# Kernel optimization log

Hardware: AMD Instinct MI355X
Metric: run time of the kernel (lower is better)

Reference implementation:

```python
import jax, jax.numpy as jnp
import numpy as np

D_K = 128
D_V = 128
SEQ_LEN = 2048


def setup_inputs() -> dict:
    key = jax.random.key(0)
    kq, kk, kv = jax.random.split(key, 3)
    q = jax.random.normal(kq, (SEQ_LEN, D_K), dtype=jnp.float32)
    k = jax.random.normal(kk, (SEQ_LEN, D_K), dtype=jnp.float32)
    v = jax.random.normal(kv, (SEQ_LEN, D_V), dtype=jnp.float32)
    return {"q": q, "k": k, "v": v}


def _step(carry, qkv):
    J, Svv, Sqv, Sqq, l = carry
    q, k, v = qkv
    l = l + 1
    fl = l.astype(J.dtype)
    # update_correlations: running means of outer products
    Svv = (fl - 1.0) / fl * Svv + jnp.outer(v, v) / fl
    Sqv = (fl - 1.0) / fl * Sqv + jnp.outer(q, v) / fl
    Sqq = (fl - 1.0) / fl * Sqq + jnp.outer(q, q) / fl

    first = l == 1

    # ecological params (J: [d_v, d_k], Sqv: [d_k, d_v], Sqq: [d_k, d_k])
    s_J = jnp.einsum('vk,kv->', J, Sqv)            # trace(J @ Sigma_qv)
    s_l = k @ Sqv @ v
    A_JJ = jnp.einsum('vk,kj,vj->', J, Sqq, J)     # trace(J Sqq J^T)
    A_ll = (v @ v) * (k @ Sqq @ k)
    A_Jl = v @ J @ Sqq @ k

    # safe denominators (unused branches must not produce NaN under where)
    A_JJ_s = jnp.where(first | (A_JJ == 0), 1.0, A_JJ)
    A_ll_s = jnp.where(first | (A_ll == 0), 1.0, A_ll)
    denom = A_JJ * A_ll - A_Jl ** 2
    denom_s = jnp.where(first | (denom == 0), 1.0, denom)

    margin = s_l - A_Jl * (s_J / A_JJ_s)

    wf = (A_ll * s_J - A_Jl * s_l) / denom_s
    wi = (A_JJ * s_l - A_Jl * s_J) / denom_s
    # nonnegativity constraints (check omega_i first, as in the source)
    wf_c = jnp.where(wi <= 0, s_J / A_JJ_s, jnp.where(wf <= 0, 0.0, wf))
    wi_c = jnp.where(wi <= 0, 0.0, jnp.where(wf <= 0, s_l / A_ll_s, wi))

    do_update = margin > 0
    vk = jnp.outer(v, k)
    J_upd = jnp.where(do_update, wf_c * J + wi_c * vk, J)
    J_new = jnp.where(first, vk, J_upd)
    updated = first | do_update

    # compute_cost with updated J and correlations
    cost = (0.5 * jnp.trace(Svv)
            - jnp.einsum('vk,kv->', J_new, Sqv)
            + 0.5 * jnp.einsum('vk,kj,vj->', J_new, Sqq, J_new))

    return (J_new, Svv, Sqv, Sqq, l), (cost, updated)


def _run(q, k, v):
    d_k, d_v = q.shape[-1], v.shape[-1]
    init = (jnp.zeros((d_v, d_k), q.dtype),
            jnp.zeros((d_v, d_v), q.dtype),
            jnp.zeros((d_k, d_v), q.dtype),
            jnp.zeros((d_k, d_k), q.dtype),
            jnp.int32(0))
    (J, _, _, _, _), (costs, updated) = jax.lax.scan(_step, init, (q, k, v))
    return costs, updated, J


def reference(q, k, v):
    return _run(q, k, v)
```

## Files before the change

### kernel.cpp

```cpp
#include <hip/hip_runtime.h>

#define SEQ 2048
#define D 128

typedef float v2f __attribute__((ext_vector_type(2)));
typedef float v4f __attribute__((ext_vector_type(4)));
#define LO2(v) __builtin_shufflevector(v, v, 0, 1)
#define HI2(v) __builtin_shufflevector(v, v, 2, 3)

__global__ __launch_bounds__(256) void precompute_kernel(
    const float* __restrict__ q, const float* __restrict__ k, const float* __restrict__ v,
    float* __restrict__ U, float* __restrict__ sl, float* __restrict__ kqq,
    float* __restrict__ vv, float* __restrict__ kq_adj, float* __restrict__ vv_adj,
    float* __restrict__ kU_adj, double* __restrict__ invl)
{
    const int s = blockIdx.x;
    const int tid = threadIdx.x;

    __shared__ float ks[D];
    __shared__ float vs[D];
    __shared__ float alpha[SEQ];
    __shared__ float red[8];
    __shared__ float upart[256];

    if (tid < D) ks[tid] = k[s * D + tid];
    else if (tid < 2 * D) vs[tid - D] = v[s * D + (tid - D)];
    __syncthreads();

    float p_a2 = 0.f, p_ab = 0.f;
    for (int i = tid; i <= s; i += 256) {
        const float4* qr = (const float4*)(q + (size_t)i * D);
        const float4* vr = (const float4*)(v + (size_t)i * D);
        float a = 0.f, b = 0.f;
#pragma unroll
        for (int j = 0; j < D / 4; ++j) {
            float4 q4 = qr[j];
            float4 v4 = vr[j];
            a += q4.x * ks[4 * j + 0] + q4.y * ks[4 * j + 1] + q4.z * ks[4 * j + 2] + q4.w * ks[4 * j + 3];
            b += v4.x * vs[4 * j + 0] + v4.y * vs[4 * j + 1] + v4.z * vs[4 * j + 2] + v4.w * vs[4 * j + 3];
        }
        alpha[i] = a;
        p_a2 += a * a;
        p_ab += a * b;
        if (i == s) vv[s] = b;
    }
#pragma unroll
    for (int off = 1; off < 64; off <<= 1) {
        p_a2 += __shfl_xor(p_a2, off);
        p_ab += __shfl_xor(p_ab, off);
    }
    const int wid = tid >> 6;
    if ((tid & 63) == 0) { red[wid] = p_a2; red[4 + wid] = p_ab; }
    __syncthreads();
    if (tid == 0) {
        kqq[s] = red[0] + red[1] + red[2] + red[3];
        sl[s]  = red[4] + red[5] + red[6] + red[7];
        invl[s] = 1.0 / (double)(s + 1);
    }

    if (tid < 64) {
        if (s + 1 < SEQ) {
            float p2 = ks[tid] * q[(size_t)(s + 1) * D + tid]
                     + ks[tid + 64] * q[(size_t)(s + 1) * D + 64 + tid];
#pragma unroll
            for (int off = 1; off < 64; off <<= 1) p2 += __shfl_xor(p2, off);
            if (tid == 0) kq_adj[s + 1] = p2;
        }
        if (s == 0 && tid == 0) { kq_adj[0] = 0.f; kU_adj[0] = 0.f; vv_adj[0] = 0.f; }
    } else if (tid < 128 && s > 0) {
        const int t2 = tid - 64;
        float p2 = vs[t2] * v[(size_t)(s - 1) * D + t2]
                 + vs[t2 + 64] * v[(size_t)(s - 1) * D + 64 + t2];
#pragma unroll
        for (int off = 1; off < 64; off <<= 1) p2 += __shfl_xor(p2, off);
        if (t2 == 0) vv_adj[s] = p2;
    }

    const int c = tid & (D - 1);
    const int h = tid >> 7;
    float a0 = 0.f, a1 = 0.f, a2 = 0.f, a3 = 0.f;
    int i = h;
    for (; i + 6 <= s; i += 8) {
        a0 = fmaf(q[(size_t)(i    ) * D + c], alpha[i    ], a0);
        a1 = fmaf(q[(size_t)(i + 2) * D + c], alpha[i + 2], a1);
        a2 = fmaf(q[(size_t)(i + 4) * D + c], alpha[i + 4], a2);
        a3 = fmaf(q[(size_t)(i + 6) * D + c], alpha[i + 6], a3);
    }
    for (; i <= s; i += 2) a0 = fmaf(q[(size_t)i * D + c], alpha[i], a0);
    upart[tid] = (a0 + a1) + (a2 + a3);
    __syncthreads();

    float kup = 0.f;
    if (tid < D) {
        const float uv = upart[tid] + upart[tid + D];
        U[(size_t)s * D + tid] = uv;
        if (s > 0) kup = uv * k[(size_t)(s - 1) * D + tid];
    }
#pragma unroll
    for (int off = 1; off < 64; off <<= 1) kup += __shfl_xor(kup, off);
    if (tid == 0)  red[0] = kup;
    if (tid == 64) red[1] = kup;
    __syncthreads();
    if (s > 0 && tid == 0) kU_adj[s] = red[0] + red[1];
}

#define DPP_ADD(x, ctrl) \
    ((x) + __int_as_float(__builtin_amdgcn_update_dpp(0, __float_as_int(x), (ctrl), 0xf, 0xf, true)))
#define REDUCE16(x) do { x = DPP_ADD(x, 0xB1); x = DPP_ADD(x, 0x4E); \
                         x = DPP_ADD(x, 0x141); x = DPP_ADD(x, 0x140); } while (0)

#define BARRIER() do { asm volatile("s_waitcnt lgkmcnt(0)" ::: "memory"); \
                       __builtin_amdgcn_s_barrier(); } while (0)

#define UPDATE_J(MODE, WF, WI)                                                \
    if ((MODE) == 2) {                                                        \
        const v2f wA = {vc4.x, vc4.x}, wB = {vc4.y, vc4.y};                   \
        const v2f wC = {vc4.z, vc4.z}, wD = {vc4.w, vc4.w};                   \
        jA0 = wA * k0_; jA1 = wA * k1_; jA2 = wA * k2_; jA3 = wA * k3_;       \
        jB0 = wB * k0_; jB1 = wB * k1_; jB2 = wB * k2_; jB3 = wB * k3_;       \
        jC0 = wC * k0_; jC1 = wC * k1_; jC2 = wC * k2_; jC3 = wC * k3_;       \
        jD0 = wD * k0_; jD1 = wD * k1_; jD2 = wD * k2_; jD3 = wD * k3_;       \
    } else if ((MODE) == 1) {                                                 \
        const v2f wf2 = {(WF), (WF)};                                         \
        const float sA = (WI) * vc4.x, sB = (WI) * vc4.y;                     \
        const float sC = (WI) * vc4.z, sD = (WI) * vc4.w;                     \
        const v2f wA = {sA, sA}, wB = {sB, sB}, wC = {sC, sC}, wD = {sD, sD}; \
        jA0 = __builtin_elementwise_fma(jA0, wf2, wA * k0_);                  \
        jA1 = __builtin_elementwise_fma(jA1, wf2, wA * k1_);                  \
        jA2 = __builtin_elementwise_fma(jA2, wf2, wA * k2_);                  \
        jA3 = __builtin_elementwise_fma(jA3, wf2, wA * k3_);                  \
        jB0 = __builtin_elementwise_fma(jB0, wf2, wB * k0_);                  \
        jB1 = __builtin_elementwise_fma(jB1, wf2, wB * k1_);                  \
        jB2 = __builtin_elementwise_fma(jB2, wf2, wB * k2_);                  \
        jB3 = __builtin_elementwise_fma(jB3, wf2, wB * k3_);                  \
        jC0 = __builtin_elementwise_fma(jC0, wf2, wC * k0_);                  \
        jC1 = __builtin_elementwise_fma(jC1, wf2, wC * k1_);                  \
        jC2 = __builtin_elementwise_fma(jC2, wf2, wC * k2_);                  \
        jC3 = __builtin_elementwise_fma(jC3, wf2, wC * k3_);                  \
        jD0 = __builtin_elementwise_fma(jD0, wf2, wD * k0_);                  \
        jD1 = __builtin_elementwise_fma(jD1, wf2, wD * k1_);                  \
        jD2 = __builtin_elementwise_fma(jD2, wf2, wD * k2_);                  \
        jD3 = __builtin_elementwise_fma(jD3, wf2, wD * k3_);                  \
    }

__global__ __launch_bounds__(1024, 4) void scan_kernel(
    const float* __restrict__ q, const float* __restrict__ k, const float* __restrict__ v,
    const float* __restrict__ U, const float* __restrict__ sl_arr,
    const float* __restrict__ kqq_arr, const float* __restrict__ vv_arr,
    const float* __restrict__ kq_adj, const float* __restrict__ vv_adj,
    const float* __restrict__ kU_adj, const double* __restrict__ invl_arr,
    float* __restrict__ out)
{
    const int tid  = threadIdx.x;
    const int lane = tid & 63;
    const int w    = __builtin_amdgcn_readfirstlane(tid >> 6);

    __shared__ float ring[3][4][160];
    __shared__ __align__(16) float wred[3][32][4];
    __shared__ __align__(16) float decLDS[3][4];

    const bool isj     = (tid >= 512);
    const int  jw      = w - 8;
    const int  i16     = lane & 15;
    const int  r4      = lane >> 4;
    const int  o       = 20 * (i16 >> 1) + 8 * (i16 & 1);
    const int  rb      = (jw << 4) + (r4 << 2);
    const int  vo      = 20 * jw + (r4 << 2);

    const bool stager  = (tid >= 128) && (tid < 512);
    const int  which   = (tid >> 7) - 1;
    const int  sidx    = tid & 127;
    const int  widx    = ((sidx >> 4) * 20) + (sidx & 15);

    const bool vstager = (tid >= 64) && (tid < 128);
    const int  s2      = tid & 63;
    const int  vc0     = 2 * s2;
    const int  vwidx   = 20 * (vc0 >> 4) + (vc0 & 15);

    v2f jA0 = {0.f, 0.f}, jA1 = jA0, jA2 = jA0, jA3 = jA0;
    v2f jB0 = jA0, jB1 = jA0, jB2 = jA0, jB3 = jA0;
    v2f jC0 = jA0, jC1 = jA0, jC2 = jA0, jC3 = jA0;
    v2f jD0 = jA0, jD1 = jA0, jD2 = jA0, jD3 = jA0;
    v4f vc4 = {0.f, 0.f, 0.f, 0.f}, vn4 = vc4;

    float gs[3] = {0.f, 0.f, 0.f};
    v2f   gv[3] = {{0.f,0.f},{0.f,0.f},{0.f,0.f}};
    float p_sl[3] = {0,0,0}, p_kq[3] = {0,0,0}, p_vv[3] = {0,0,0};
    float p_kqa[3] = {0,0,0}, p_vva[3] = {0,0,0}, p_vvp[3] = {0,0,0};
    float p_kua[3] = {0,0,0};
    double p_inv[3] = {0,0,0};

    if (stager) {
        if (which == 0) {
            ring[0][0][widx] = q[(size_t)1 * D + sidx];
            ring[1][0][widx] = q[(size_t)2 * D + sidx];
            gs[2] = q[(size_t)3 * D + sidx];
            gs[0] = q[(size_t)4 * D + sidx];
            gs[1] = q[(size_t)5 * D + sidx];
        } else if (which == 1) {
            ring[0][1][widx] = U[(size_t)1 * D + sidx];
            ring[1][1][widx] = U[(size_t)2 * D + sidx];
            gs[2] = U[(size_t)3 * D + sidx];
            gs[0] = U[(size_t)4 * D + sidx];
            gs[1] = U[(size_t)5 * D + sidx];
        } else {
            ring[0][2][widx] = k[sidx];
            ring[1][2][widx] = k[(size_t)1 * D + sidx];
            gs[2] = k[(size_t)2 * D + sidx];
            gs[0] = k[(size_t)3 * D + sidx];
            gs[1] = k[(size_t)4 * D + sidx];
        }
    } else if (vstager) {
        *(v2f*)&ring[0][3][vwidx] = *(const v2f*)&v[(size_t)1 * D + vc0];
        *(v2f*)&ring[1][3][vwidx] = *(const v2f*)&v[(size_t)2 * D + vc0];
        gv[2] = *(const v2f*)&v[(size_t)3 * D + vc0];
        gv[0] = *(const v2f*)&v[(size_t)4 * D + vc0];
        gv[1] = *(const v2f*)&v[(size_t)5 * D + vc0];
    } else if (isj) {
        vc4 = *(const v4f*)&v[rb];
    }

    float dwf = 0.f, dwi = 1.f;
    int dmode = 2;
    if (tid == 0) { decLDS[0][0] = 0.f; decLDS[0][1] = 1.f; decLDS[0][2] = 2.f; decLDS[0][3] = 0.f; }

    double SJ = 0.0, AJJ = 0.0, trSvv = 0.0;
    if (w == 0) {
        p_sl[0]  = sl_arr[1];  p_kq[0]  = kqq_arr[1]; p_vv[0] = vv_arr[1];
        p_kqa[0] = kq_adj[1];  p_vva[0] = vv_adj[1];  p_kua[0] = kU_adj[1];
        p_inv[0] = invl_arr[1]; p_vvp[0] = vv_arr[0];
        p_sl[1]  = sl_arr[2];  p_kq[1]  = kqq_arr[2]; p_vv[1] = vv_arr[2];
        p_kqa[1] = kq_adj[2];  p_vva[1] = vv_adj[2];  p_kua[1] = kU_adj[2];
        p_inv[1] = invl_arr[2]; p_vvp[1] = vv_arr[1];

        const double sl0 = (double)sl_arr[0];
        const double kq0 = (double)kqq_arr[0];
        const double vv0 = (double)vv_arr[0];
        trSvv = vv0;
        SJ  = sl0;
        AJJ = vv0 * kq0;
        if (lane == 0) {
            out[0] = (float)((0.5 * trSvv - SJ + 0.5 * AJJ) * invl_arr[0]);
            out[SEQ] = 1.f;
        }
    }
    BARRIER();

#define STEP_BODY(I, P, PN, PW)                                               \
{                                                                             \
    v2f k0_ = {0.f, 0.f}, k1_ = k0_, k2_ = k0_, k3_ = k0_;                    \
    if (isj) {                                                                \
        const v4f Qa = ((const v4f*)&ring[P][0][o])[0];                       \
        const v4f Qb = ((const v4f*)&ring[P][0][o])[1];                       \
        const v4f Ua = ((const v4f*)&ring[P][1][o])[0];                       \
        const v4f Ub = ((const v4f*)&ring[P][1][o])[1];                       \
        const v4f Ka = ((const v4f*)&ring[P][2][o])[0];                       \
        const v4f Kb = ((const v4f*)&ring[P][2][o])[1];                       \
        vn4 = *((const v4f*)&ring[P][3][vo]);                                 \
        k0_ = LO2(Ka); k1_ = HI2(Ka); k2_ = LO2(Kb); k3_ = HI2(Kb);           \
        const v2f q0 = LO2(Qa), q1 = HI2(Qa), q2 = LO2(Qb), q3 = HI2(Qb);     \
        v2f aA = jA0 * q0, aB = jB0 * q0, aC = jC0 * q0, aD = jD0 * q0;       \
        aA = __builtin_elementwise_fma(jA1, q1, aA);                          \
        aB = __builtin_elementwise_fma(jB1, q1, aB);                          \
        aC = __builtin_elementwise_fma(jC1, q1, aC);                          \
        aD = __builtin_elementwise_fma(jD1, q1, aD);                          \
        aA = __builtin_elementwise_fma(jA2, q2, aA);                          \
        aB = __builtin_elementwise_fma(jB2, q2, aB);                          \
        aC = __builtin_elementwise_fma(jC2, q2, aC);                          \
        aD = __builtin_elementwise_fma(jD2, q2, aD);                          \
        aA = __builtin_elementwise_fma(jA3, q3, aA);                          \
        aB = __builtin_elementwise_fma(jB3, q3, aB);                          \
        aC = __builtin_elementwise_fma(jC3, q3, aC);                          \
        aD = __builtin_elementwise_fma(jD3, q3, aD);                          \
        float YqA = aA.x + aA.y, YqB = aB.x + aB.y;                           \
        float YqC = aC.x + aC.y, YqD = aD.x + aD.y;                           \
        const v2f u0 = LO2(Ua), u1 = HI2(Ua), u2 = LO2(Ub), u3 = HI2(Ub);     \
        v2f bA = jA0 * u0, bB = jB0 * u0, bC = jC0 * u0, bD = jD0 * u0;       \
        bA = __builtin_elementwise_fma(jA1, u1, bA);                          \
        bB = __builtin_elementwise_fma(jB1, u1, bB);                          \
        bC = __builtin_elementwise_fma(jC1, u1, bC);                          \
        bD = __builtin_elementwise_fma(jD1, u1, bD);                          \
        bA = __builtin_elementwise_fma(jA2, u2, bA);                          \
        bB = __builtin_elementwise_fma(jB2, u2, bB);                          \
        bC = __builtin_elementwise_fma(jC2, u2, bC);                          \
        bD = __builtin_elementwise_fma(jD2, u2, bD);                          \
        bA = __builtin_elementwise_fma(jA3, u3, bA);                          \
        bB = __builtin_elementwise_fma(jB3, u3, bB);                          \
        bC = __builtin_elementwise_fma(jC3, u3, bC);                          \
        bD = __builtin_elementwise_fma(jD3, u3, bD);                          \
        float YwA = bA.x + bA.y, YwB = bB.x + bB.y;                           \
        float YwC = bC.x + bC.y, YwD = bD.x + bD.y;                           \
        REDUCE16(YqA); REDUCE16(YqB); REDUCE16(YqC); REDUCE16(YqD);           \
        REDUCE16(YwA); REDUCE16(YwB); REDUCE16(YwC); REDUCE16(YwD);           \
        const float z1 = (vn4.x * YqA + vn4.y * YqB) + (vn4.z * YqC + vn4.w * YqD); \
        const float z2 = (YqA * YqA + YqB * YqB) + (YqC * YqC + YqD * YqD);   \
        const float z3 = (vc4.x * YqA + vc4.y * YqB) + (vc4.z * YqC + vc4.w * YqD); \
        const float z4 = (vn4.x * YwA + vn4.y * YwB) + (vn4.z * YwC + vn4.w * YwD); \
        if ((lane & 15) == 15)                                                \
            *(float4*)&wred[P][(jw << 2) | r4][0] = make_float4(z1, z2, z3, z4); \
    } else if (w == 0) {                                                      \
        const int t_ = ((I) + 3 < SEQ) ? (I) + 3 : SEQ - 1;                   \
        p_sl[PW]  = sl_arr[t_];   p_kq[PW]  = kqq_arr[t_];                    \
        p_vv[PW]  = vv_arr[t_];   p_kqa[PW] = kq_adj[t_];                     \
        p_vva[PW] = vv_adj[t_];   p_kua[PW] = kU_adj[t_];                     \
        p_inv[PW] = invl_arr[t_]; p_vvp[PW] = p_vv[PN];                       \
    }                                                                         \
    BARRIER();                                                                \
    if (stager) {                                                             \
        ring[PW][which][widx] = gs[PW];                                       \
        const int tq_ = ((I) + 6 < SEQ) ? (I) + 6 : SEQ - 1;                  \
        const int tk_ = ((I) + 5 < SEQ) ? (I) + 5 : SEQ - 1;                  \
        gs[PW] = (which == 0) ? q[(size_t)tq_ * D + sidx]                     \
               : (which == 1) ? U[(size_t)tq_ * D + sidx]                     \
                              : k[(size_t)tk_ * D + sidx];                    \
    } else if (vstager) {                                                     \
        *(v2f*)&ring[PW][3][vwidx] = gv[PW];                                  \
        const int tv_ = ((I) + 6 < SEQ) ? (I) + 6 : SEQ - 1;                  \
        gv[PW] = *(const v2f*)&v[(size_t)tv_ * D + vc0];                      \
    } else if (isj) {                                                         \
        const float4 df = *(const float4*)&decLDS[P][0];                      \
        const float uwf = df.x, uwi = df.y;                                   \
        const int   umode = (int)df.z;                                        \
        UPDATE_J(umode, uwf, uwi)                                             \
        vc4 = vn4;                                                            \
    } else if (w == 0) {                                                      \
        const float c_sl  = p_sl[P],  c_kq  = p_kq[P],  c_vv  = p_vv[P];      \
        const float c_kqa = p_kqa[P], c_vva = p_vva[P], c_vvp = p_vvp[P];     \
        const float c_kua = p_kua[P];                                         \
        const double c_inv = p_inv[P];                                        \
        const float4 wa = *(const float4*)&wred[P][lane & 15][0];             \
        const float4 wb = *(const float4*)&wred[P][16 + (lane & 15)][0];      \
        float4 ww = make_float4(wa.x + wb.x, wa.y + wb.y,                     \
                                wa.z + wb.z, wa.w + wb.w);                    \
        const float odwf = dwf, odwi = dwi;                                   \
        const int   odmode = dmode;                                           \
        REDUCE16(ww.x);                                                       \
        REDUCE16(ww.y);                                                       \
        REDUCE16(ww.z);                                                       \
        REDUCE16(ww.w);                                                       \
        double a_, b_;                                                        \
        if (odmode == 2)      { a_ = 0.0; b_ = 1.0; }                         \
        else if (odmode == 1) { a_ = (double)odwf; b_ = (double)odwi; }       \
        else                  { a_ = 1.0; b_ = 0.0; }                         \
        const double kqa = (double)c_kqa, vva = (double)c_vva;                \
        const double vvp = (double)c_vvp, kua = (double)c_kua;                \
        const double r1 = (double)ww.x, r2 = (double)ww.y;                    \
        const double r3 = (double)ww.z, r4_ = (double)ww.w;                   \
        const double Jqv  = a_ * r1 + b_ * (kqa * vva);                       \
        const double Jq2  = a_ * a_ * r2 + 2.0 * a_ * b_ * kqa * r3          \
                          + b_ * b_ * kqa * kqa * vvp;                        \
        const double AJl_ = a_ * r4_ + b_ * kua * vva;                        \
        trSvv += (double)c_vv;                                                \
        SJ    += Jqv;                                                         \
        AJJ   += Jq2;                                                         \
        const double s_l  = (double)c_sl;                                     \
        const double A_ll = (double)c_vv * (double)c_kq;                      \
        const double AJJ_s  = (AJJ == 0.0)  ? 1.0 : AJJ;                      \
        const double A_ll_s = (A_ll == 0.0) ? 1.0 : A_ll;                     \
        const double divJ = SJ / AJJ_s;     \
        const double divL = s_l / A_ll_s;   \
        const double denom   = AJJ * A_ll - AJl_ * AJl_;                      \
        const double denom_s = (denom == 0.0) ? 1.0 : denom;                  \
        const double rden = 1.0 / denom_s;                                    \
        const double wf = (A_ll * SJ - AJl_ * s_l) * rden;                    \
        const double wi = (AJJ * s_l - AJl_ * SJ) * rden;                     \
        double wf_c, wi_c;                                                    \
        if (wi <= 0.0)      { wf_c = divJ; wi_c = 0.0; }                      \
        else if (wf <= 0.0) { wf_c = 0.0;  wi_c = divL; }                     \
        else                { wf_c = wf;   wi_c = wi; }                       \
        const bool do_update = (s_l * AJJ_s - AJl_ * SJ) > 0.0;               \
        int mode;                                                             \
        if (do_update) {                                                      \
            mode = 1;                                                         \
            const double nSJ = wf_c * SJ + wi_c * s_l;                        \
            AJJ = wf_c * wf_c * AJJ + 2.0 * wf_c * wi_c * AJl_                \
                + wi_c * wi_c * A_ll;                                         \
            SJ = nSJ;                                                         \
        } else {                                                              \
            mode = 0;                                                         \
        }                                                                     \
        dwf = (float)wf_c; dwi = (float)wi_c; dmode = mode;                   \
        if (lane == 0) {                                                      \
            out[(I) + 1] = (float)((0.5 * trSvv - SJ + 0.5 * AJJ) * c_inv);   \
            out[SEQ + (I) + 1] = mode ? 1.f : 0.f;                            \
            *(float4*)&decLDS[PN][0] = make_float4(dwf, dwi, (float)mode, 0.f);\
        }                                                                     \
    }                                                                         \
}

    for (int i = 0; i + 2 < SEQ - 1; i += 3) {
        STEP_BODY(i,     0, 1, 2)
        STEP_BODY(i + 1, 1, 2, 0)
        STEP_BODY(i + 2, 2, 0, 1)
    }
    STEP_BODY(SEQ - 2, 0, 1, 2)
#undef STEP_BODY

    BARRIER();
    if (isj) {
        const float4 df = *(const float4*)&decLDS[1][0];
        const float fwf = df.x, fwi = df.y;
        const int   fmode = (int)df.z;
        const v4f Ka = ((const v4f*)&ring[1][2][o])[0];
        const v4f Kb = ((const v4f*)&ring[1][2][o])[1];
        const v2f k0_ = LO2(Ka), k1_ = HI2(Ka), k2_ = LO2(Kb), k3_ = HI2(Kb);
        UPDATE_J(fmode, fwf, fwi)
        float* jb = out + 2 * SEQ + (size_t)rb * D + 8 * i16;
        *(v4f*)(jb + 0)         = __builtin_shufflevector(jA0, jA1, 0, 1, 2, 3);
        *(v4f*)(jb + 4)         = __builtin_shufflevector(jA2, jA3, 0, 1, 2, 3);
        *(v4f*)(jb + D + 0)     = __builtin_shufflevector(jB0, jB1, 0, 1, 2, 3);
        *(v4f*)(jb + D + 4)     = __builtin_shufflevector(jB2, jB3, 0, 1, 2, 3);
        *(v4f*)(jb + 2 * D + 0) = __builtin_shufflevector(jC0, jC1, 0, 1, 2, 3);
        *(v4f*)(jb + 2 * D + 4) = __builtin_shufflevector(jC2, jC3, 0, 1, 2, 3);
        *(v4f*)(jb + 3 * D + 0) = __builtin_shufflevector(jD0, jD1, 0, 1, 2, 3);
        *(v4f*)(jb + 3 * D + 4) = __builtin_shufflevector(jD2, jD3, 0, 1, 2, 3);
    }
}

extern "C" void kernel_launch(void* const* d_in, const int* in_sizes, int n_in,
                              void* d_out, int out_size, void* d_ws, size_t ws_size,
                              hipStream_t stream) {
    (void)in_sizes; (void)n_in; (void)out_size; (void)ws_size;
    const float* q = (const float*)d_in[0];
    const float* k = (const float*)d_in[1];
    const float* v = (const float*)d_in[2];
    float* out = (float*)d_out;

    float* U      = (float*)d_ws;
    float* sl     = U + (size_t)SEQ * D;
    float* kqq    = sl + SEQ;
    float* vv     = kqq + SEQ;
    float* kq_adj = vv + SEQ;
    float* vv_adj = kq_adj + SEQ;
    float* kU_adj = vv_adj + SEQ;
    double* invl  = (double*)(kU_adj + SEQ);

    precompute_kernel<<<SEQ, 256, 0, stream>>>(q, k, v, U, sl, kqq, vv,
                                               kq_adj, vv_adj, kU_adj, invl);
    scan_kernel<<<1, 1024, 0, stream>>>(q, k, v, U, sl, kqq, vv,
                                        kq_adj, vv_adj, kU_adj, invl, out);
}
```

Before: 2.615 ms.

## Compute scalar decision redundantly in all J waves and update J immediately

Instead of wave 0 computing the per-step scalar decision and publishing it through LDS for the J waves to apply one step later, every J wave now reduces the partial sums itself, runs the double-precision decision, and applies the J update in the same step. The J update is applied eagerly, so the reductions already see the updated J and the adjustment terms (kq_adj, vv_adj, kU_adj) are dropped. The per-step scalar inputs are preloaded into LDS at kernel start, and a sched_barrier is added after each barrier. This removes a cross-wave handoff and one pipeline stage per step, at the cost of redundant double-precision math in all eight J waves and more LDS.

Result: no change. 2.606 ms (-0.3%).

```diff
diff --git a/kernel.cpp b/kernel.cpp
--- a/kernel.cpp
+++ b/kernel.cpp
@@ -110,38 +110,8 @@
                          x = DPP_ADD(x, 0x141); x = DPP_ADD(x, 0x140); } while (0)
 
 #define BARRIER() do { asm volatile("s_waitcnt lgkmcnt(0)" ::: "memory"); \
-                       __builtin_amdgcn_s_barrier(); } while (0)
-
-#define UPDATE_J(MODE, WF, WI)                                                \
-    if ((MODE) == 2) {                                                        \
-        const v2f wA = {vc4.x, vc4.x}, wB = {vc4.y, vc4.y};                   \
-        const v2f wC = {vc4.z, vc4.z}, wD = {vc4.w, vc4.w};                   \
-        jA0 = wA * k0_; jA1 = wA * k1_; jA2 = wA * k2_; jA3 = wA * k3_;       \
-        jB0 = wB * k0_; jB1 = wB * k1_; jB2 = wB * k2_; jB3 = wB * k3_;       \
-        jC0 = wC * k0_; jC1 = wC * k1_; jC2 = wC * k2_; jC3 = wC * k3_;       \
-        jD0 = wD * k0_; jD1 = wD * k1_; jD2 = wD * k2_; jD3 = wD * k3_;       \
-    } else if ((MODE) == 1) {                                                 \
-        const v2f wf2 = {(WF), (WF)};                                         \
-        const float sA = (WI) * vc4.x, sB = (WI) * vc4.y;                     \
-        const float sC = (WI) * vc4.z, sD = (WI) * vc4.w;                     \
-        const v2f wA = {sA, sA}, wB = {sB, sB}, wC = {sC, sC}, wD = {sD, sD}; \
-        jA0 = __builtin_elementwise_fma(jA0, wf2, wA * k0_);                  \
-        jA1 = __builtin_elementwise_fma(jA1, wf2, wA * k1_);                  \
-        jA2 = __builtin_elementwise_fma(jA2, wf2, wA * k2_);                  \
-        jA3 = __builtin_elementwise_fma(jA3, wf2, wA * k3_);                  \
-        jB0 = __builtin_elementwise_fma(jB0, wf2, wB * k0_);                  \
-        jB1 = __builtin_elementwise_fma(jB1, wf2, wB * k1_);                  \
-        jB2 = __builtin_elementwise_fma(jB2, wf2, wB * k2_);                  \
-        jB3 = __builtin_elementwise_fma(jB3, wf2, wB * k3_);                  \
-        jC0 = __builtin_elementwise_fma(jC0, wf2, wC * k0_);                  \
-        jC1 = __builtin_elementwise_fma(jC1, wf2, wC * k1_);                  \
-        jC2 = __builtin_elementwise_fma(jC2, wf2, wC * k2_);                  \
-        jC3 = __builtin_elementwise_fma(jC3, wf2, wC * k3_);                  \
-        jD0 = __builtin_elementwise_fma(jD0, wf2, wD * k0_);                  \
-        jD1 = __builtin_elementwise_fma(jD1, wf2, wD * k1_);                  \
-        jD2 = __builtin_elementwise_fma(jD2, wf2, wD * k2_);                  \
-        jD3 = __builtin_elementwise_fma(jD3, wf2, wD * k3_);                  \
-    }
+                       __builtin_amdgcn_s_barrier(); \
+                       __builtin_amdgcn_sched_barrier(0); } while (0)
 
 __global__ __launch_bounds__(1024, 4) void scan_kernel(
     const float* __restrict__ q, const float* __restrict__ k, const float* __restrict__ v,
@@ -154,10 +124,14 @@
     const int tid  = threadIdx.x;
     const int lane = tid & 63;
     const int w    = __builtin_amdgcn_readfirstlane(tid >> 6);
+    (void)kq_adj; (void)vv_adj; (void)kU_adj;
 
     __shared__ float ring[3][4][160];
     __shared__ __align__(16) float wred[3][32][4];
-    __shared__ __align__(16) float decLDS[3][4];
+    __shared__ __align__(16) float fsl[SEQ];
+    __shared__ __align__(16) float fkq[SEQ];
+    __shared__ __align__(16) float fvv[SEQ];
+    __shared__ __align__(16) double finv[SEQ];
 
     const bool isj     = (tid >= 512);
     const int  jw      = w - 8;
@@ -181,14 +155,17 @@
     v2f jB0 = jA0, jB1 = jA0, jB2 = jA0, jB3 = jA0;
     v2f jC0 = jA0, jC1 = jA0, jC2 = jA0, jC3 = jA0;
     v2f jD0 = jA0, jD1 = jA0, jD2 = jA0, jD3 = jA0;
-    v4f vc4 = {0.f, 0.f, 0.f, 0.f}, vn4 = vc4;
 
     float gs[3] = {0.f, 0.f, 0.f};
     v2f   gv[3] = {{0.f,0.f},{0.f,0.f},{0.f,0.f}};
-    float p_sl[3] = {0,0,0}, p_kq[3] = {0,0,0}, p_vv[3] = {0,0,0};
-    float p_kqa[3] = {0,0,0}, p_vva[3] = {0,0,0}, p_vvp[3] = {0,0,0};
-    float p_kua[3] = {0,0,0};
-    double p_inv[3] = {0,0,0};
+
+    if (tid < 512) {
+        ((float4*)fsl)[tid] = ((const float4*)sl_arr)[tid];
+        ((float4*)fvv)[tid] = ((const float4*)vv_arr)[tid];
+    } else {
+        ((float4*)fkq)[tid - 512] = ((const float4*)kqq_arr)[tid - 512];
+    }
+    ((double2*)finv)[tid] = ((const double2*)invl_arr)[tid];
 
     if (stager) {
         if (which == 0) {
@@ -204,11 +181,11 @@
             gs[0] = U[(size_t)4 * D + sidx];
             gs[1] = U[(size_t)5 * D + sidx];
         } else {
-            ring[0][2][widx] = k[sidx];
-            ring[1][2][widx] = k[(size_t)1 * D + sidx];
-            gs[2] = k[(size_t)2 * D + sidx];
-            gs[0] = k[(size_t)3 * D + sidx];
-            gs[1] = k[(size_t)4 * D + sidx];
+            ring[0][2][widx] = k[(size_t)1 * D + sidx];
+            ring[1][2][widx] = k[(size_t)2 * D + sidx];
+            gs[2] = k[(size_t)3 * D + sidx];
+            gs[0] = k[(size_t)4 * D + sidx];
+            gs[1] = k[(size_t)5 * D + sidx];
         }
     } else if (vstager) {
         *(v2f*)&ring[0][3][vwidx] = *(const v2f*)&v[(size_t)1 * D + vc0];
@@ -216,40 +193,43 @@
         gv[2] = *(const v2f*)&v[(size_t)3 * D + vc0];
         gv[0] = *(const v2f*)&v[(size_t)4 * D + vc0];
         gv[1] = *(const v2f*)&v[(size_t)5 * D + vc0];
-    } else if (isj) {
-        vc4 = *(const v4f*)&v[rb];
-    }
-
-    float dwf = 0.f, dwi = 1.f;
-    int dmode = 2;
-    if (tid == 0) { decLDS[0][0] = 0.f; decLDS[0][1] = 1.f; decLDS[0][2] = 2.f; decLDS[0][3] = 0.f; }
+    }
 
     double SJ = 0.0, AJJ = 0.0, trSvv = 0.0;
-    if (w == 0) {
-        p_sl[0]  = sl_arr[1];  p_kq[0]  = kqq_arr[1]; p_vv[0] = vv_arr[1];
-        p_kqa[0] = kq_adj[1];  p_vva[0] = vv_adj[1];  p_kua[0] = kU_adj[1];
-        p_inv[0] = invl_arr[1]; p_vvp[0] = vv_arr[0];
-        p_sl[1]  = sl_arr[2];  p_kq[1]  = kqq_arr[2]; p_vv[1] = vv_arr[2];
-        p_kqa[1] = kq_adj[2];  p_vva[1] = vv_adj[2];  p_kua[1] = kU_adj[2];
-        p_inv[1] = invl_arr[2]; p_vvp[1] = vv_arr[1];
-
+    if (isj) {
+        const v4f v0  = *(const v4f*)&v[rb];
+        const v4f Ka0 = *(const v4f*)&k[8 * i16];
+        const v4f Kb0 = *(const v4f*)&k[8 * i16 + 4];
+        const v2f k0_ = LO2(Ka0), k1_ = HI2(Ka0), k2_ = LO2(Kb0), k3_ = HI2(Kb0);
+        const v2f wA = {v0.x, v0.x}, wB = {v0.y, v0.y};
+        const v2f wC = {v0.z, v0.z}, wD = {v0.w, v0.w};
+        jA0 = wA * k0_; jA1 = wA * k1_; jA2 = wA * k2_; jA3 = wA * k3_;
+        jB0 = wB * k0_; jB1 = wB * k1_; jB2 = wB * k2_; jB3 = wB * k3_;
+        jC0 = wC * k0_; jC1 = wC * k1_; jC2 = wC * k2_; jC3 = wC * k3_;
+        jD0 = wD * k0_; jD1 = wD * k1_; jD2 = wD * k2_; jD3 = wD * k3_;
+        const double vv0 = (double)vv_arr[0];
+        SJ    = (double)sl_arr[0];
+        AJJ   = vv0 * (double)kqq_arr[0];
+        trSvv = vv0;
+    }
+    if (tid == 0) {
         const double sl0 = (double)sl_arr[0];
         const double kq0 = (double)kqq_arr[0];
         const double vv0 = (double)vv_arr[0];
-        trSvv = vv0;
-        SJ  = sl0;
-        AJJ = vv0 * kq0;
-        if (lane == 0) {
-            out[0] = (float)((0.5 * trSvv - SJ + 0.5 * AJJ) * invl_arr[0]);
-            out[SEQ] = 1.f;
-        }
-    }
-    BARRIER();
+        out[0] = (float)((0.5 * vv0 - sl0 + 0.5 * vv0 * kq0) * invl_arr[0]);
+        out[SEQ] = 1.f;
+    }
+    __syncthreads();
 
 #define STEP_BODY(I, P, PN, PW)                                               \
 {                                                                             \
+    float c_sl = 0.f, c_kq = 0.f, c_vv = 0.f;                                 \
+    double c_inv = 0.0;                                                       \
     v2f k0_ = {0.f, 0.f}, k1_ = k0_, k2_ = k0_, k3_ = k0_;                    \
+    v4f vn4 = {0.f, 0.f, 0.f, 0.f};                                           \
     if (isj) {                                                                \
+        c_sl = fsl[(I) + 1]; c_kq = fkq[(I) + 1]; c_vv = fvv[(I) + 1];        \
+        c_inv = finv[(I) + 1];                                                \
         const v4f Qa = ((const v4f*)&ring[P][0][o])[0];                       \
         const v4f Qb = ((const v4f*)&ring[P][0][o])[1];                       \
         const v4f Ua = ((const v4f*)&ring[P][1][o])[0];                       \
@@ -294,96 +274,83 @@
         REDUCE16(YwA); REDUCE16(YwB); REDUCE16(YwC); REDUCE16(YwD);           \
         const float z1 = (vn4.x * YqA + vn4.y * YqB) + (vn4.z * YqC + vn4.w * YqD); \
         const float z2 = (YqA * YqA + YqB * YqB) + (YqC * YqC + YqD * YqD);   \
-        const float z3 = (vc4.x * YqA + vc4.y * YqB) + (vc4.z * YqC + vc4.w * YqD); \
         const float z4 = (vn4.x * YwA + vn4.y * YwB) + (vn4.z * YwC + vn4.w * YwD); \
         if ((lane & 15) == 15)                                                \
-            *(float4*)&wred[P][(jw << 2) | r4][0] = make_float4(z1, z2, z3, z4); \
-    } else if (w == 0) {                                                      \
-        const int t_ = ((I) + 3 < SEQ) ? (I) + 3 : SEQ - 1;                   \
-        p_sl[PW]  = sl_arr[t_];   p_kq[PW]  = kqq_arr[t_];                    \
-        p_vv[PW]  = vv_arr[t_];   p_kqa[PW] = kq_adj[t_];                     \
-        p_vva[PW] = vv_adj[t_];   p_kua[PW] = kU_adj[t_];                     \
-        p_inv[PW] = invl_arr[t_]; p_vvp[PW] = p_vv[PN];                       \
+            *(float4*)&wred[P][(jw << 2) | r4][0] = make_float4(z1, z2, z4, 0.f); \
     }                                                                         \
     BARRIER();                                                                \
     if (stager) {                                                             \
         ring[PW][which][widx] = gs[PW];                                       \
-        const int tq_ = ((I) + 6 < SEQ) ? (I) + 6 : SEQ - 1;                  \
-        const int tk_ = ((I) + 5 < SEQ) ? (I) + 5 : SEQ - 1;                  \
-        gs[PW] = (which == 0) ? q[(size_t)tq_ * D + sidx]                     \
-               : (which == 1) ? U[(size_t)tq_ * D + sidx]                     \
-                              : k[(size_t)tk_ * D + sidx];                    \
+        const int t6 = ((I) + 6 < SEQ) ? (I) + 6 : SEQ - 1;                   \
+        gs[PW] = (which == 0) ? q[(size_t)t6 * D + sidx]                      \
+               : (which == 1) ? U[(size_t)t6 * D + sidx]                      \
+                              : k[(size_t)t6 * D + sidx];                     \
     } else if (vstager) {                                                     \
         *(v2f*)&ring[PW][3][vwidx] = gv[PW];                                  \
-        const int tv_ = ((I) + 6 < SEQ) ? (I) + 6 : SEQ - 1;                  \
-        gv[PW] = *(const v2f*)&v[(size_t)tv_ * D + vc0];                      \
+        const int t6 = ((I) + 6 < SEQ) ? (I) + 6 : SEQ - 1;                   \
+        gv[PW] = *(const v2f*)&v[(size_t)t6 * D + vc0];                       \
     } else if (isj) {                                                         \
-        const float4 df = *(const float4*)&decLDS[P][0];                      \
-        const float uwf = df.x, uwi = df.y;                                   \
-        const int   umode = (int)df.z;                                        \
-        UPDATE_J(umode, uwf, uwi)                                             \
-        vc4 = vn4;                                                            \
-    } else if (w == 0) {                                                      \
-        const float c_sl  = p_sl[P],  c_kq  = p_kq[P],  c_vv  = p_vv[P];      \
-        const float c_kqa = p_kqa[P], c_vva = p_vva[P], c_vvp = p_vvp[P];     \
-        const float c_kua = p_kua[P];                                         \
-        const double c_inv = p_inv[P];                                        \
         const float4 wa = *(const float4*)&wred[P][lane & 15][0];             \
         const float4 wb = *(const float4*)&wred[P][16 + (lane & 15)][0];      \
-        float4 ww = make_float4(wa.x + wb.x, wa.y + wb.y,                     \
-                                wa.z + wb.z, wa.w + wb.w);                    \
-        const float odwf = dwf, odwi = dwi;                                   \
-        const int   odmode = dmode;                                           \
-        REDUCE16(ww.x);                                                       \
-        REDUCE16(ww.y);                                                       \
-        REDUCE16(ww.z);                                                       \
-        REDUCE16(ww.w);                                                       \
-        double a_, b_;                                                        \
-        if (odmode == 2)      { a_ = 0.0; b_ = 1.0; }                         \
-        else if (odmode == 1) { a_ = (double)odwf; b_ = (double)odwi; }       \
-        else                  { a_ = 1.0; b_ = 0.0; }                         \
-        const double kqa = (double)c_kqa, vva = (double)c_vva;                \
-        const double vvp = (double)c_vvp, kua = (double)c_kua;                \
-        const double r1 = (double)ww.x, r2 = (double)ww.y;                    \
-        const double r3 = (double)ww.z, r4_ = (double)ww.w;                   \
-        const double Jqv  = a_ * r1 + b_ * (kqa * vva);                       \
-        const double Jq2  = a_ * a_ * r2 + 2.0 * a_ * b_ * kqa * r3          \
-                          + b_ * b_ * kqa * kqa * vvp;                        \
-        const double AJl_ = a_ * r4_ + b_ * kua * vva;                        \
+        float wx = wa.x + wb.x, wy = wa.y + wb.y, wz = wa.z + wb.z;           \
+        REDUCE16(wx);                                                         \
+        REDUCE16(wy);                                                         \
+        REDUCE16(wz);                                                         \
         trSvv += (double)c_vv;                                                \
-        SJ    += Jqv;                                                         \
-        AJJ   += Jq2;                                                         \
+        SJ    += (double)wx;                                                  \
+        AJJ   += (double)wy;                                                  \
+        const double AJl_ = (double)wz;                                       \
         const double s_l  = (double)c_sl;                                     \
         const double A_ll = (double)c_vv * (double)c_kq;                      \
         const double AJJ_s  = (AJJ == 0.0)  ? 1.0 : AJJ;                      \
         const double A_ll_s = (A_ll == 0.0) ? 1.0 : A_ll;                     \
-        const double divJ = SJ / AJJ_s;     \
-        const double divL = s_l / A_ll_s;   \
         const double denom   = AJJ * A_ll - AJl_ * AJl_;                      \
         const double denom_s = (denom == 0.0) ? 1.0 : denom;                  \
         const double rden = 1.0 / denom_s;                                    \
         const double wf = (A_ll * SJ - AJl_ * s_l) * rden;                    \
         const double wi = (AJJ * s_l - AJl_ * SJ) * rden;                     \
         double wf_c, wi_c;                                                    \
-        if (wi <= 0.0)      { wf_c = divJ; wi_c = 0.0; }                      \
-        else if (wf <= 0.0) { wf_c = 0.0;  wi_c = divL; }                     \
-        else                { wf_c = wf;   wi_c = wi; }                       \
+        if (wi <= 0.0)      { wf_c = SJ / AJJ_s;  wi_c = 0.0; }               \
+        else if (wf <= 0.0) { wf_c = 0.0;         wi_c = s_l / A_ll_s; }      \
+        else                { wf_c = wf;          wi_c = wi; }                \
         const bool do_update = (s_l * AJJ_s - AJl_ * SJ) > 0.0;               \
-        int mode;                                                             \
+        int mode = 0;                                                         \
         if (do_update) {                                                      \
             mode = 1;                                                         \
             const double nSJ = wf_c * SJ + wi_c * s_l;                        \
             AJJ = wf_c * wf_c * AJJ + 2.0 * wf_c * wi_c * AJl_                \
                 + wi_c * wi_c * A_ll;                                         \
             SJ = nSJ;                                                         \
-        } else {                                                              \
-            mode = 0;                                                         \
+            const float uwf = (float)wf_c;                                    \
+            const float uwi = (float)wi_c;                                    \
+            const v2f wf2 = {uwf, uwf};                                       \
+            const float sA = uwi * vn4.x, sB = uwi * vn4.y;                   \
+            const float sC = uwi * vn4.z, sD = uwi * vn4.w;                   \
+            const v2f wA = {sA, sA}, wB = {sB, sB};                           \
+            const v2f wC = {sC, sC}, wD = {sD, sD};                           \
+            jA0 = __builtin_elementwise_fma(jA0, wf2, wA * k0_);              \
+            jA1 = __builtin_elementwise_fma(jA1, wf2, wA * k1_);              \
+            jA2 = __builtin_elementwise_fma(jA2, wf2, wA * k2_);              \
+            jA3 = __builtin_elementwise_fma(jA3, wf2, wA * k3_);              \
+            jB0 = __builtin_elementwise_fma(jB0, wf2, wB * k0_);              \
+            jB1 = __builtin_elementwise_fma(jB1, wf2, wB * k1_);              \
+            jB2 = __builtin_elementwise_fma(jB2, wf2, wB * k2_);              \
+            jB3 = __builtin_elementwise_fma(jB3, wf2, wB * k3_);              \
+            jC0 = __builtin_elementwise_fma(jC0, wf2, wC * k0_);              \
+            jC1 = __builtin_elementwise_fma(jC1, wf2, wC * k1_);              \
+            jC2 = __builtin_elementwise_fma(jC2, wf2, wC * k2_);              \
+            jC3 = __builtin_elementwise_fma(jC3, wf2, wC * k3_);              \
+            jD0 = __builtin_elementwise_fma(jD0, wf2, wD * k0_);              \
+            jD1 = __builtin_elementwise_fma(jD1, wf2, wD * k1_);              \
+            jD2 = __builtin_elementwise_fma(jD2, wf2, wD * k2_);              \
+            jD3 = __builtin_elementwise_fma(jD3, wf2, wD * k3_);              \
         }                                                                     \
-        dwf = (float)wf_c; dwi = (float)wi_c; dmode = mode;                   \
-        if (lane == 0) {                                                      \
-            out[(I) + 1] = (float)((0.5 * trSvv - SJ + 0.5 * AJJ) * c_inv);   \
-            out[SEQ + (I) + 1] = mode ? 1.f : 0.f;                            \
-            *(float4*)&decLDS[PN][0] = make_float4(dwf, dwi, (float)mode, 0.f);\
+        if (w == 8) {                                                         \
+            const float cost = (float)((0.5 * trSvv - SJ + 0.5 * AJJ) * c_inv); \
+            if (lane == 0) {                                                  \
+                out[(I) + 1] = cost;                                          \
+                out[SEQ + (I) + 1] = mode ? 1.f : 0.f;                        \
+            }                                                                 \
         }                                                                     \
     }                                                                         \
 }
@@ -396,15 +363,7 @@
     STEP_BODY(SEQ - 2, 0, 1, 2)
 #undef STEP_BODY
 
-    BARRIER();
     if (isj) {
-        const float4 df = *(const float4*)&decLDS[1][0];
-        const float fwf = df.x, fwi = df.y;
-        const int   fmode = (int)df.z;
-        const v4f Ka = ((const v4f*)&ring[1][2][o])[0];
-        const v4f Kb = ((const v4f*)&ring[1][2][o])[1];
-        const v2f k0_ = LO2(Ka), k1_ = HI2(Ka), k2_ = LO2(Kb), k3_ = HI2(Kb);
-        UPDATE_J(fmode, fwf, fwi)
         float* jb = out + 2 * SEQ + (size_t)rb * D + 8 * i16;
         *(v4f*)(jb + 0)         = __builtin_shufflevector(jA0, jA1, 0, 1, 2, 3);
         *(v4f*)(jb + 4)         = __builtin_shufflevector(jA2, jA3, 0, 1, 2, 3);
```
